# Performance work log

Hardware: AMD Instinct MI355X
Metric: run time of the kernel (lower is better)

Reference implementation:

```python
import jax, jax.numpy as jnp
import numpy as np

RECALL_THRESHOLD = 0.3
LAMBDA_PAUC = 0.5
NUM_CLASSES = 128
LABEL_SMOOTHING = 0.1
N_SAMPLES = 131072


def setup_inputs() -> dict:
    key = jax.random.key(0)
    k1, k2 = jax.random.split(key)
    predictions = jax.random.normal(k1, (N_SAMPLES, NUM_CLASSES), dtype=jnp.float32)
    targets = jax.random.randint(k2, (N_SAMPLES,), 0, NUM_CLASSES)
    return {"predictions": predictions, "targets": targets}


def _macro_pauc(probs, targets):
    """Vectorized (over classes) partial AUC at max_fpr = 1 - recall_threshold.

    Equivalent to the per-class torch loop: descending argsort of scores,
    cumsum TP/FP, clip the ROC curve at max_fpr with linear interpolation of
    the crossing segment, trapezoidal integration, macro-average over classes
    that have at least one positive.
    """
    N, K = probs.shape
    order = jnp.argsort(-probs, axis=0)                      # [N, K] descending per class
    t_sorted = (targets[order] == jnp.arange(K)[None, :]).astype(probs.dtype)  # [N, K]
    tps = jnp.cumsum(t_sorted, axis=0)                        # [N, K]
    fps = jnp.cumsum(1.0 - t_sorted, axis=0)                  # [N, K]
    tpr = tps / jnp.maximum(tps[-1], 1.0)
    fpr = fps / jnp.maximum(fps[-1], 1.0)

    max_fpr = 1.0 - RECALL_THRESHOLD
    # Clip fpr at max_fpr; segments fully beyond the cut get delta == 0 so
    # their tpr value is irrelevant. The crossing segment's right endpoint is
    # replaced by the linearly interpolated tpr at max_fpr (matches torch's
    # slope-based interpolation with the same 1e-8 guard).
    fpr_c = jnp.minimum(fpr, max_fpr)
    slope = (tpr[1:] - tpr[:-1]) / (fpr[1:] - fpr[:-1] + 1e-8)
    tpr_interp = tpr[:-1] + slope * (max_fpr - fpr[:-1])
    tpr_next = jnp.where(fpr[1:] <= max_fpr, tpr[1:], tpr_interp)
    delta = fpr_c[1:] - fpr_c[:-1]                            # [N-1, K]
    pauc_c = jnp.sum(delta * 0.5 * (tpr_next + tpr[:-1]), axis=0)  # [K]

    valid = (tps[-1] > 0).astype(probs.dtype)                 # macro: skip empty classes
    return jnp.sum(pauc_c * valid) / jnp.maximum(jnp.sum(valid), 1.0)


def reference(predictions, targets):
    logp = jax.nn.log_softmax(predictions, axis=1)
    probs = jnp.exp(logp)
    # CrossEntropyLoss with label smoothing (mean reduction, no class weights):
    # loss_i = (1-eps) * nll_i + eps * mean_c(-log p_ic)
    nll = -jnp.take_along_axis(logp, targets[:, None], axis=1)[:, 0]
    smooth = -jnp.mean(logp, axis=1)
    ce_loss = jnp.mean((1.0 - LABEL_SMOOTHING) * nll + LABEL_SMOOTHING * smooth)

    # torch.tensor(pauc) in the original detaches pAUC from the graph.
    pauc = jax.lax.stop_gradient(_macro_pauc(probs, targets))
    pauc_loss = 1.0 - pauc ** 2
    return (1.0 - LAMBDA_PAUC) * ce_loss + LAMBDA_PAUC * pauc_loss
```

## Files before the change

### kernel.cpp

```cpp
#include <hip/hip_runtime.h>
#include <math.h>

#define N_SAMPLES 131072
#define NUM_CLASSES 128
#define NB 256
#define MAX_FPR 0.7f
#define NBLK 256
#define ROWS_PER_BLK 512
#define HPITCH 129
#define PART_WORDS (NUM_CLASSES * 128)

typedef unsigned long long u64;
typedef unsigned int u32;

__device__ __forceinline__ int bin_of(float x, float off ) {
    int b = (int)__fmaf_rn(x, 16.0f, off);
    return min(max(b, 0), NB - 1);
}

__global__ __launch_bounds__(1024, 4) void fused_kernel(
    const float* __restrict__ pred, const int* __restrict__ tgt,
    u32* __restrict__ hPos,
    u32* __restrict__ part,
    float* __restrict__ acc)
{
    __shared__ u32 h32[NUM_CLASSES * HPITCH];
    __shared__ float wsum[16];

    const int tid  = threadIdx.x;
    const int w    = tid >> 6;
    const int lane = tid & 63;
    const int j    = lane & 15;
    const int rs   = lane >> 4;

    for (int i = tid; i < NUM_CLASSES * HPITCH; i += 1024) h32[i] = 0u;
    __syncthreads();

    const int rowBase = blockIdx.x * ROWS_PER_BLK + w * 4 + rs;
    float acc_lse = 0.0f, acc_xt = 0.0f, acc_sx = 0.0f;

    const float* r0p = pred + (size_t)rowBase * 128;
    float4 a0 = *(const float4*)(r0p + j * 4);
    float4 a1 = *(const float4*)(r0p + 64 + j * 4);
    int    ta = tgt[rowBase];
    const float* r1p = r0p + (size_t)64 * 128;
    float4 c0 = *(const float4*)(r1p + j * 4);
    float4 c1 = *(const float4*)(r1p + 64 + j * 4);
    int    tb = tgt[rowBase + 64];

    #pragma unroll
    for (int p = 0; p < 8; p++) {
        float4 n0, n1; int tn = 0;
        if (p < 6) {
            const float* rn = pred + (size_t)(rowBase + (p + 2) * 64) * 128;
            n0 = *(const float4*)(rn + j * 4);
            n1 = *(const float4*)(rn + 64 + j * 4);
            tn = tgt[rowBase + (p + 2) * 64];
        }

        float e = __expf(a0.x) + __expf(a0.y) + __expf(a0.z) + __expf(a0.w)
                + __expf(a1.x) + __expf(a1.y) + __expf(a1.z) + __expf(a1.w);
        #pragma unroll
        for (int o = 1; o < 16; o <<= 1) e += __shfl_xor(e, o);
        const float lse = __logf(e);
        const float off = (14.0f - lse) * 16.0f;

        const float xv[8] = {a0.x, a0.y, a0.z, a0.w, a1.x, a1.y, a1.z, a1.w};
        #pragma unroll
        for (int q = 0; q < 8; q++) {
            const int c = (q < 4) ? (j * 4 + q) : (64 + j * 4 + (q - 4));
            const int b = bin_of(xv[q], off);
            const int word = ((b >> 1) + j) & 127;
            atomicAdd(&h32[c * HPITCH + word], (b & 1) ? 65536u : 1u);
        }

        acc_sx  += (xv[0] + xv[1] + xv[2] + xv[3])
                 + (xv[4] + xv[5] + xv[6] + xv[7]);
        acc_lse += lse * 0.0625f;

        {
            const int t = ta;
            float xt; bool hit = false;
            if ((t >> 2) == j)                        { xt = xv[t & 3];       hit = true; }
            else if (t >= 64 && ((t - 64) >> 2) == j) { xt = xv[4 + (t & 3)]; hit = true; }
            if (hit) {
                acc_xt += xt;
                atomicAdd(&hPos[(t << 8) | bin_of(xt, off)], 1u);
            }
        }

        a0 = c0; a1 = c1; ta = tb;
        c0 = n0; c1 = n1; tb = tn;
    }

    float ce = acc_lse - 0.9f * acc_xt - (0.1f / 128.0f) * acc_sx;
    #pragma unroll
    for (int o = 32; o; o >>= 1) ce += __shfl_xor(ce, o);
    if (lane == 0) wsum[w] = ce;
    __syncthreads();
    if (tid == 0) {
        float s = 0.0f;
        #pragma unroll
        for (int i = 0; i < 16; i++) s += wsum[i];
        atomicAdd(&acc[0], s);
    }

    u32* outp = part + (size_t)blockIdx.x * PART_WORDS;
    for (int i = tid; i < PART_WORDS; i += 1024) {
        const int c = i >> 7, bw = i & 127;
        outp[i] = h32[c * HPITCH + ((bw + ((c >> 2) & 15)) & 127)];
    }
}

__global__ __launch_bounds__(256) void pauc_reduce(
    const u32* __restrict__ part,
    const u32* __restrict__ hPos,
    float* __restrict__ acc,
    float* __restrict__ out)
{
    __shared__ __align__(16) u32 sA[NB];

    const int k    = blockIdx.x;
    const int t    = threadIdx.x;
    const int w    = t & 127;
    const int half = t >> 7;

    u32 lo = 0u, hi = 0u;
    const u32* p0 = part + (size_t)(half * (NBLK / 2)) * PART_WORDS
                         + k * 128 + w;
    #pragma unroll 8
    for (int b = 0; b < NBLK / 2; b++) {
        const u32 q = p0[(size_t)b * PART_WORDS];
        lo += q & 0xffffu; hi += q >> 16;
    }
    if (half == 0) { sA[2 * w] = lo; sA[2 * w + 1] = hi; }
    __syncthreads();
    if (half == 1) { sA[2 * w] += lo; sA[2 * w + 1] += hi; }
    __syncthreads();

    if (t < 64) {
        const int lane = t;
        const uint4 q  = ((const uint4*)sA)[63 - lane];
        const u32 a[4] = {q.w, q.z, q.y, q.x};
        const uint4 pq = ((const uint4*)(hPos + (k << 8)))[63 - lane];
        const u32 p[4] = {pq.w, pq.z, pq.y, pq.x};

        const u32 la = a[0] + a[1] + a[2] + a[3];
        const u32 lp = p[0] + p[1] + p[2] + p[3];

        u32 ia = la, ip = lp;
        #pragma unroll
        for (int o = 1; o < 64; o <<= 1) {
            const u32 tA = __shfl_up(ia, o);
            const u32 tP = __shfl_up(ip, o);
            if (lane >= o) { ia += tA; ip += tP; }
        }
        const u32 P = __shfl(ip, 63);
        const u32 T = __shfl(ia, 63);
        const float Pm = fmaxf((float)P, 1.0f);
        const float Fm = fmaxf((float)(T - P), 1.0f);

        int cumA = (int)(ia - la), cumP = (int)(ip - lp);
        float contrib = 0.0f;
        #pragma unroll
        for (int i = 0; i < 4; i++) {
            const int f = (int)a[i] - (int)p[i];
            if (f > 0) {
                const float fpr0 = (float)(cumA - cumP) / Fm;
                if (fpr0 < MAX_FPR) {
                    const float tpr0 = (float)cumP / Pm;
                    const float tpr1 = (float)(cumP + (int)p[i]) / Pm;
                    const float fpr1 = (float)(cumA - cumP + f) / Fm;
                    if (fpr1 <= MAX_FPR) {
                        contrib += (fpr1 - fpr0) * 0.5f * (tpr0 + tpr1);
                    } else {
                        const float tfrac = (MAX_FPR - fpr0) / (fpr1 - fpr0);
                        const float tprc  = tpr0 + tfrac * (tpr1 - tpr0);
                        contrib += (MAX_FPR - fpr0) * 0.5f * (tpr0 + tprc);
                    }
                }
            }
            cumA += (int)a[i]; cumP += (int)p[i];
        }

        #pragma unroll
        for (int o = 32; o; o >>= 1) contrib += __shfl_xor(contrib, o);

        if (lane == 0) {
            if (P > 0u) {
                atomicAdd(&acc[1], contrib);
                atomicAdd(&acc[2], 1.0f);
            }
            __threadfence();
            const u32 done = atomicAdd((u32*)(acc + 3), 1u);
            if (done == NUM_CLASSES - 1) {
                const float ces = atomicAdd(&acc[0], 0.0f);
                const float ps  = atomicAdd(&acc[1], 0.0f);
                const float vs  = atomicAdd(&acc[2], 0.0f);
                const float cem  = ces * (1.0f / (float)N_SAMPLES);
                const float pauc = ps / fmaxf(vs, 1.0f);
                out[0] = 0.5f * cem + 0.5f * (1.0f - pauc * pauc);
            }
        }
    }
}

extern "C" void kernel_launch(void* const* d_in, const int* in_sizes, int n_in,
                              void* d_out, int out_size, void* d_ws, size_t ws_size,
                              hipStream_t stream)
{
    const float* pred = (const float*)d_in[0];
    const int*   tgt  = (const int*)d_in[1];

    char* ws = (char*)d_ws;
    u32*   hPos = (u32*)ws;
    float* acc  = (float*)(ws + 131072);
    u32*   part = (u32*)(ws + 262144);

    hipMemsetAsync(ws, 0, 131072 + 32, stream);

    fused_kernel<<<NBLK, 1024, 0, stream>>>(pred, tgt, hPos, part, acc);
    pauc_reduce<<<NUM_CLASSES, 256, 0, stream>>>(part, hPos, acc, (float*)d_out);
}
```

Baseline: 111.1 us.

## Double block count, map 8 lanes per row, and load all rows upfront

Uses twice as many blocks with half the rows each and assigns 8 lanes per row, with 16 elements per lane. Each thread now handles two rows loaded at once, replacing the rolling software-pipelined loop, and the word-rotation swizzle on the shared histogram is removed. The goal is more parallelism and memory-level parallelism across the GPU. The cost is twice as many partial histograms to write and reduce, and likely more LDS bank conflicts without the swizzle. The unchanged reduce kernel reads part with NBLK/2 per half, so it follows the new block count.

```diff
diff --git a/kernel.cpp b/kernel.cpp
--- a/kernel.cpp
+++ b/kernel.cpp
@@ -5,8 +5,8 @@
 #define NUM_CLASSES 128
 #define NB 256
 #define MAX_FPR 0.7f
-#define NBLK 256
-#define ROWS_PER_BLK 512
+#define NBLK 512
+#define ROWS_PER_BLK 256
 #define HPITCH 129
 #define PART_WORDS (NUM_CLASSES * 128)
 
@@ -18,7 +18,42 @@
     return min(max(b, 0), NB - 1);
 }
 
-__global__ __launch_bounds__(1024, 4) void fused_kernel(
+__device__ __forceinline__ void do_pass(
+    float4 a0, float4 a1, float4 a2, float4 a3, int t, int j,
+    u32* h32, u32* __restrict__ hPos,
+    float& acc_lse, float& acc_xt, float& acc_sx)
+{
+    const float xv[16] = {a0.x, a0.y, a0.z, a0.w, a1.x, a1.y, a1.z, a1.w,
+                          a2.x, a2.y, a2.z, a2.w, a3.x, a3.y, a3.z, a3.w};
+    float e = 0.0f;
+    #pragma unroll
+    for (int q = 0; q < 16; q++) e += __expf(xv[q]);
+    #pragma unroll
+    for (int o = 1; o < 8; o <<= 1) e += __shfl_xor(e, o);
+    const float lse = __logf(e);
+    const float off = (14.0f - lse) * 16.0f;
+
+    #pragma unroll
+    for (int q = 0; q < 16; q++) {
+        const int c = ((q >> 2) << 5) + (j << 2) + (q & 3);
+        const int b = bin_of(xv[q], off);
+        atomicAdd(&h32[c * HPITCH + (b >> 1)], (b & 1) ? 65536u : 1u);
+    }
+
+    float sx = 0.0f;
+    #pragma unroll
+    for (int q = 0; q < 16; q++) sx += xv[q];
+    acc_sx += sx;
+    if (j == 0) acc_lse += lse;
+
+    if (((t & 31) >> 2) == j) {
+        const float xt = xv[((t >> 5) << 2) + (t & 3)];
+        acc_xt += xt;
+        atomicAdd(&hPos[(t << 8) | bin_of(xt, off)], 1u);
+    }
+}
+
+__global__ __launch_bounds__(1024, 8) void fused_kernel(
     const float* __restrict__ pred, const int* __restrict__ tgt,
     u32* __restrict__ hPos,
     u32* __restrict__ part,
@@ -30,68 +65,31 @@
     const int tid  = threadIdx.x;
     const int w    = tid >> 6;
     const int lane = tid & 63;
-    const int j    = lane & 15;
-    const int rs   = lane >> 4;
+    const int j    = lane & 7;
+    const int rs   = lane >> 3;
 
     for (int i = tid; i < NUM_CLASSES * HPITCH; i += 1024) h32[i] = 0u;
     __syncthreads();
 
-    const int rowBase = blockIdx.x * ROWS_PER_BLK + w * 4 + rs;
+    const int row0 = blockIdx.x * ROWS_PER_BLK + w * 8 + rs;
+    const int row1 = row0 + 128;
+
+    const float* rp0 = pred + (size_t)row0 * 128 + j * 4;
+    const float* rp1 = pred + (size_t)row1 * 128 + j * 4;
+    const float4 a0 = *(const float4*)(rp0);
+    const float4 a1 = *(const float4*)(rp0 + 32);
+    const float4 a2 = *(const float4*)(rp0 + 64);
+    const float4 a3 = *(const float4*)(rp0 + 96);
+    const float4 b0 = *(const float4*)(rp1);
+    const float4 b1 = *(const float4*)(rp1 + 32);
+    const float4 b2 = *(const float4*)(rp1 + 64);
+    const float4 b3 = *(const float4*)(rp1 + 96);
+    const int t0 = tgt[row0];
+    const int t1 = tgt[row1];
+
     float acc_lse = 0.0f, acc_xt = 0.0f, acc_sx = 0.0f;
-
-    const float* r0p = pred + (size_t)rowBase * 128;
-    float4 a0 = *(const float4*)(r0p + j * 4);
-    float4 a1 = *(const float4*)(r0p + 64 + j * 4);
-    int    ta = tgt[rowBase];
-    const float* r1p = r0p + (size_t)64 * 128;
-    float4 c0 = *(const float4*)(r1p + j * 4);
-    float4 c1 = *(const float4*)(r1p + 64 + j * 4);
-    int    tb = tgt[rowBase + 64];
-
-    #pragma unroll
-    for (int p = 0; p < 8; p++) {
-        float4 n0, n1; int tn = 0;
-        if (p < 6) {
-            const float* rn = pred + (size_t)(rowBase + (p + 2) * 64) * 128;
-            n0 = *(const float4*)(rn + j * 4);
-            n1 = *(const float4*)(rn + 64 + j * 4);
-            tn = tgt[rowBase + (p + 2) * 64];
-        }
-
-        float e = __expf(a0.x) + __expf(a0.y) + __expf(a0.z) + __expf(a0.w)
-                + __expf(a1.x) + __expf(a1.y) + __expf(a1.z) + __expf(a1.w);
-        #pragma unroll
-        for (int o = 1; o < 16; o <<= 1) e += __shfl_xor(e, o);
-        const float lse = __logf(e);
-        const float off = (14.0f - lse) * 16.0f;
-
-        const float xv[8] = {a0.x, a0.y, a0.z, a0.w, a1.x, a1.y, a1.z, a1.w};
-        #pragma unroll
-        for (int q = 0; q < 8; q++) {
-            const int c = (q < 4) ? (j * 4 + q) : (64 + j * 4 + (q - 4));
-            const int b = bin_of(xv[q], off);
-            const int word = ((b >> 1) + j) & 127;
-            atomicAdd(&h32[c * HPITCH + word], (b & 1) ? 65536u : 1u);
-        }
-
-        acc_sx  += (xv[0] + xv[1] + xv[2] + xv[3])
-                 + (xv[4] + xv[5] + xv[6] + xv[7]);
-        acc_lse += lse * 0.0625f;
-
-        {
-            const int t = ta;
-            float xt; bool hit = false;
-            if ((t >> 2) == j)                        { xt = xv[t & 3];       hit = true; }
-            else if (t >= 64 && ((t - 64) >> 2) == j) { xt = xv[4 + (t & 3)]; hit = true; }
-            if (hit) {
-                acc_xt += xt;
-                atomicAdd(&hPos[(t << 8) | bin_of(xt, off)], 1u);
-            }
-        }
-
-        a0 = c0; a1 = c1; ta = tb;
-        c0 = n0; c1 = n1; tb = tn;
-    }
+    do_pass(a0, a1, a2, a3, t0, j, h32, hPos, acc_lse, acc_xt, acc_sx);
+    do_pass(b0, b1, b2, b3, t1, j, h32, hPos, acc_lse, acc_xt, acc_sx);
 
     float ce = acc_lse - 0.9f * acc_xt - (0.1f / 128.0f) * acc_sx;
     #pragma unroll
@@ -106,10 +104,8 @@
     }
 
     u32* outp = part + (size_t)blockIdx.x * PART_WORDS;
-    for (int i = tid; i < PART_WORDS; i += 1024) {
-        const int c = i >> 7, bw = i & 127;
-        outp[i] = h32[c * HPITCH + ((bw + ((c >> 2) & 15)) & 127)];
-    }
+    for (int i = tid; i < PART_WORDS; i += 1024)
+        outp[i] = h32[(i >> 7) * HPITCH + (i & 127)];
 }
 
 __global__ __launch_bounds__(256) void pauc_reduce(
```

Measured after the change: 120.3 us. +8.2%, slower.
